# Optimization experiments

Measured on AMD Instinct MI355X. Metric: run time of the kernel, lower is better.

The kernel has to match this reference:

```python
import jax, jax.numpy as jnp
import numpy as np

ALPHA = 0.2
WINDOW = 64
HEADS = 2

def _mhsa(x, qkv_W, qkv_b, out_W, out_b):
    # x: (M, w, C)
    M, w, C = x.shape
    hd = C // HEADS
    qkv = (x @ qkv_W + qkv_b).reshape(M, w, 3, HEADS, hd)
    q, k, v = qkv[:, :, 0], qkv[:, :, 1], qkv[:, :, 2]  # (M, w, H, hd)
    att = jnp.einsum('mqhd,mkhd->mhqk', q, k) * (hd ** -0.5)
    att = jax.nn.softmax(att, axis=-1)
    o = jnp.einsum('mhqk,mkhd->mqhd', att, v).reshape(M, w, C)
    return o @ out_W + out_b

def _block_pass(x, qkv_W, qkv_b, out_W, out_b):
    # x: (B*L, L, C) -> windowed attention along axis 1
    BL, L, C = x.shape
    pad = (-L) % WINDOW
    if pad > 0:
        x = jnp.pad(x, ((0, 0), (0, pad), (0, 0)))
    Lp = L + pad
    nblk = Lp // WINDOW
    xb = x.reshape(BL * nblk, WINDOW, C)
    xb = _mhsa(xb, qkv_W, qkv_b, out_W, out_b)
    return xb.reshape(BL, Lp, C)[:, :L, :]

def setup_inputs() -> dict:
    key = jax.random.key(0)
    ks = jax.random.split(key, 12)
    s = 0.02
    d = {
        'single': jax.random.normal(ks[0], (1, 512, 256), jnp.float32),
        'pair': jax.random.normal(ks[1], (1, 512, 512, 128), jnp.float32),
        'film_W1': jax.random.normal(ks[2], (512, 128), jnp.float32) * s,
        'film_b1': jnp.zeros((128,), jnp.float32),
        'film_W2': jax.random.normal(ks[3], (128, 256), jnp.float32) * s,
        'film_b2': jnp.zeros((256,), jnp.float32),
        'red_W1': jax.random.normal(ks[4], (128, 64), jnp.float32) * s,
        'red_b1': jnp.zeros((64,), jnp.float32),
        'red_W2': jax.random.normal(ks[5], (64, 32), jnp.float32) * s,
        'red_b2': jnp.zeros((32,), jnp.float32),
        'qkv_W': jax.random.normal(ks[6], (32, 96), jnp.float32) * s,
        'qkv_b': jnp.zeros((96,), jnp.float32),
        'out_W': jax.random.normal(ks[7], (32, 32), jnp.float32) * s,
        'out_b': jnp.zeros((32,), jnp.float32),
        'head_W1': jax.random.normal(ks[8], (32, 64), jnp.float32) * s,
        'head_b1': jnp.zeros((64,), jnp.float32),
        'head_W2': jax.random.normal(ks[9], (64, 1), jnp.float32) * s,
        'head_b2': jnp.zeros((1,), jnp.float32),
    }
    return d

def reference(single, pair, film_W1, film_b1, film_W2, film_b2,
              red_W1, red_b1, red_W2, red_b2,
              qkv_W, qkv_b, out_W, out_b,
              head_W1, head_b1, head_W2, head_b2):
    B, L, Ds = single.shape
    pair_dim = pair.shape[-1]
    # ResidualFiLM: concat([Si,Sj]) @ W1 == Si @ W1[:Ds] + Sj @ W1[Ds:]
    pi = single @ film_W1[:Ds]   # (B, L, hidden)
    pj = single @ film_W1[Ds:]   # (B, L, hidden)
    h = jax.nn.relu(pi[:, :, None, :] + pj[:, None, :, :] + film_b1)  # (B,L,L,hidden)
    x = h @ film_W2 + film_b2    # (B,L,L,2*pair_dim)
    gamma = 1.0 + ALPHA * jnp.tanh(x[..., :pair_dim])
    beta = ALPHA * jnp.tanh(x[..., pair_dim:])
    pair2 = gamma * pair + beta
    # pair_reduce: Linear -> GELU(exact) -> Linear
    pair2 = jax.nn.gelu(pair2 @ red_W1 + red_b1, approximate=False) @ red_W2 + red_b2  # (B,L,L,32)
    C = pair2.shape[-1]
    # row pass
    row = _block_pass(pair2.reshape(B * L, L, C), qkv_W, qkv_b, out_W, out_b)
    row = row.reshape(B, L, L, C)
    # col pass (attend along first L axis)
    col = _block_pass(row.transpose(0, 2, 1, 3).reshape(B * L, L, C), qkv_W, qkv_b, out_W, out_b)
    pair3 = col.reshape(B, L, L, C).transpose(0, 2, 1, 3)
    # head
    logits = (jax.nn.relu(pair3 @ head_W1 + head_b1) @ head_W2 + head_b2)[..., 0]
    return jax.nn.sigmoid(logits)  # (B,L,L)
```

## Files before the change

### kernel.cpp

```cpp
#include <hip/hip_runtime.h>
#include <hip/hip_bf16.h>
#include <math.h>

typedef unsigned short u16;
typedef u16 u16x8 __attribute__((ext_vector_type(8)));
typedef u16 u16x4 __attribute__((ext_vector_type(4)));
typedef __bf16 bf16x8 __attribute__((ext_vector_type(8)));
typedef float f32x4 __attribute__((ext_vector_type(4)));

__device__ __forceinline__ u16 f2bf(float f) {
    return __builtin_bit_cast(u16, (__bf16)f);
}
__device__ __forceinline__ float ftanh(float x) {
    const float e = __expf(2.f * x);
    return 1.f - 2.f * __builtin_amdgcn_rcpf(e + 1.f);
}
__device__ __forceinline__ float fgelu(float x) {
    const float u = 0.7978845608028654f * x * (1.f + 0.044715f * x * x);
    return 0.5f * x * (1.f + ftanh(u));
}

#define MFMA16(A, B, C) __builtin_amdgcn_mfma_f32_16x16x32_bf16( \
    __builtin_bit_cast(bf16x8, A), __builtin_bit_cast(bf16x8, B), C, 0, 0, 0)

#define BARRIER() do { \
    asm volatile("s_waitcnt lgkmcnt(0)" ::: "memory"); \
    __builtin_amdgcn_s_barrier(); \
    __builtin_amdgcn_sched_barrier(0); \
} while (0)

__global__ __launch_bounds__(256) void k_prep(
    const float* __restrict__ fW2, const float* __restrict__ rW1,
    const float* __restrict__ rW2, const float* __restrict__ qW,
    const float* __restrict__ oW,
    u16* __restrict__ W2T, u16* __restrict__ rW1T, u16* __restrict__ rW2T,
    u16* __restrict__ qWT, u16* __restrict__ oWT)
{
    const int idx = blockIdx.x * 256 + threadIdx.x;
    if (idx < 256 * 128) {
        const int c = idx >> 7, k = idx & 127;
        W2T[idx] = f2bf(fW2[k * 256 + c]);
    }
    const int i2 = idx - 32768;
    if (i2 >= 0 && i2 < 64 * 128) {
        const int d = i2 >> 7, k = i2 & 127;
        rW1T[i2] = f2bf(rW1[k * 64 + d]);
    }
    const int i3 = idx - 40960;
    if (i3 >= 0 && i3 < 32 * 64) {
        const int e = i3 >> 6, d = i3 & 63;
        rW2T[i3] = f2bf(rW2[d * 32 + e]);
    }
    const int i4 = idx - 43008;
    if (i4 >= 0 && i4 < 96 * 32) {
        const int col = i4 >> 5, c = i4 & 31;
        qWT[i4] = f2bf(qW[c * 96 + col]);
    }
    const int i5 = idx - 46080;
    if (i5 >= 0 && i5 < 32 * 32) {
        const int oc = i5 >> 5, d = i5 & 31;
        oWT[i5] = f2bf(oW[d * 32 + oc]);
    }
}

__global__ __launch_bounds__(256) void k_pipj(const float* __restrict__ single,
                                              const float* __restrict__ fW1,
                                              const float* __restrict__ fb1,
                                              float* __restrict__ pi,
                                              float* __restrict__ pj) {
    const int i = blockIdx.x;
    const int t = threadIdx.x;
    const int sel = t >> 7;
    const int c = t & 127;
    const float* srow = single + i * 256;
    const float* w = fW1 + sel * 256 * 128 + c;
    float acc = 0.f;
    for (int k = 0; k < 256; ++k) acc += srow[k] * w[k * 128];
    if (sel == 0) acc += fb1[c];
    float* dst = sel ? pj : pi;
    dst[i * 128 + c] = acc;
}

__global__ __launch_bounds__(256) void k_film_red_mfma(
    const float* __restrict__ pair,
    const float* __restrict__ pi,
    const float* __restrict__ pj,
    const u16*   __restrict__ W2T,
    const float* __restrict__ fb2,
    const u16*   __restrict__ rW1T,
    const float* __restrict__ rb1,
    const u16*   __restrict__ rW2T,
    const float* __restrict__ rb2,
    float* __restrict__ out)
{
    __shared__ __align__(16) char hs [32 * 256];
    __shared__ __align__(16) char p2s[32 * 256];
    __shared__ __align__(16) char t1s[32 * 128];

    const int t = threadIdx.x;
    const int lane = t & 63, w = t >> 6;
    const int g = lane >> 4, ln = lane & 15;
    const int i = blockIdx.x >> 4;
    const int j0 = (blockIdx.x & 15) * 32;

    const int jj = t >> 3;
    const int k0 = (t & 7) * 16;
    const float* pir = pi + i * 128 + k0;
    const float* pjr = pj + (j0 + jj) * 128 + k0;
    f32x4 pv[4], qv[4];
#pragma unroll
    for (int q4 = 0; q4 < 4; ++q4) {
        pv[q4] = *(const f32x4*)(pir + 4 * q4);
        qv[q4] = *(const f32x4*)(pjr + 4 * q4);
    }

    u16x8 af1[4][4];
#pragma unroll
    for (int a = 0; a < 4; ++a)
#pragma unroll
        for (int ks = 0; ks < 4; ++ks)
            af1[a][ks] = *(const u16x8*)(W2T + ((w + 4 * a) * 16 + ln) * 128 + ks * 32 + g * 8);

    f32x4 pr[2][2];
#pragma unroll
    for (int a2 = 0; a2 < 2; ++a2)
#pragma unroll
        for (int nt = 0; nt < 2; ++nt) {
            const int j = nt * 16 + ln;
            const int c0 = (w + 4 * a2) * 16 + g * 4;
            pr[a2][nt] = *(const f32x4*)(pair + ((long)(i * 512 + j0 + j)) * 128 + c0);
        }

    {
        u16x8 pk0, pk1;
#pragma unroll
        for (int e = 0; e < 8; ++e) {
            const float v0 = pv[e >> 2][e & 3] + qv[e >> 2][e & 3];
            const float v1 = pv[2 + (e >> 2)][e & 3] + qv[2 + (e >> 2)][e & 3];
            pk0[e] = f2bf(fmaxf(v0, 0.f));
            pk1[e] = f2bf(fmaxf(v1, 0.f));
        }
        const int sw = (jj & 7) << 4;
        *(u16x8*)(hs + jj * 256 + ((2 * k0) ^ sw)) = pk0;
        *(u16x8*)(hs + jj * 256 + ((2 * (k0 + 8)) ^ sw)) = pk1;
    }
    BARRIER();

    f32x4 acc[4][2] = {};
#pragma unroll
    for (int ks = 0; ks < 4; ++ks) {
        u16x8 b0, b1;
        {
            const int jA = ln, jB = 16 + ln;
            const int k = ks * 32 + g * 8;
            b0 = *(const u16x8*)(hs + jA * 256 + ((2 * k) ^ ((jA & 7) << 4)));
            b1 = *(const u16x8*)(hs + jB * 256 + ((2 * k) ^ ((jB & 7) << 4)));
        }
#pragma unroll
        for (int a = 0; a < 4; ++a) {
            acc[a][0] = MFMA16(af1[a][ks], b0, acc[a][0]);
            acc[a][1] = MFMA16(af1[a][ks], b1, acc[a][1]);
        }
    }

    u16x8 af2[4];
#pragma unroll
    for (int ks = 0; ks < 4; ++ks)
        af2[ks] = *(const u16x8*)(rW1T + (w * 16 + ln) * 128 + ks * 32 + g * 8);

#pragma unroll
    for (int a2 = 0; a2 < 2; ++a2) {
        const int c0 = (w + 4 * a2) * 16 + g * 4;
        const f32x4 blo = *(const f32x4*)(fb2 + c0);
        const f32x4 bhi = *(const f32x4*)(fb2 + 128 + c0);
#pragma unroll
        for (int nt = 0; nt < 2; ++nt) {
            u16x4 pb;
#pragma unroll
            for (int r = 0; r < 4; ++r) {
                const float xlo = acc[a2][nt][r] + blo[r];
                const float xhi = acc[a2 + 2][nt][r] + bhi[r];
                const float gam = 1.f + 0.2f * ftanh(xlo);
                const float bet = 0.2f * ftanh(xhi);
                pb[r] = f2bf(gam * pr[a2][nt][r] + bet);
            }
            const int j = nt * 16 + ln;
            *(u16x4*)(p2s + j * 256 + ((2 * c0) ^ ((j & 7) << 4))) = pb;
        }
    }
    BARRIER();

    const int mt3 = w >> 1, nt3 = w & 1;
    u16x8 a3[2];
#pragma unroll
    for (int ks = 0; ks < 2; ++ks)
        a3[ks] = *(const u16x8*)(rW2T + (mt3 * 16 + ln) * 64 + ks * 32 + g * 8);

    f32x4 acc2[2] = {};
#pragma unroll
    for (int ks = 0; ks < 4; ++ks) {
        const int k = ks * 32 + g * 8;
        const int jA = ln, jB = 16 + ln;
        const u16x8 b0 = *(const u16x8*)(p2s + jA * 256 + ((2 * k) ^ ((jA & 7) << 4)));
        const u16x8 b1 = *(const u16x8*)(p2s + jB * 256 + ((2 * k) ^ ((jB & 7) << 4)));
        acc2[0] = MFMA16(af2[ks], b0, acc2[0]);
        acc2[1] = MFMA16(af2[ks], b1, acc2[1]);
    }

    {
        const int d0 = w * 16 + g * 4;
        const f32x4 rb = *(const f32x4*)(rb1 + d0);
#pragma unroll
        for (int nt = 0; nt < 2; ++nt) {
            u16x4 tb;
#pragma unroll
            for (int r = 0; r < 4; ++r)
                tb[r] = f2bf(fgelu(acc2[nt][r] + rb[r]));
            const int j = nt * 16 + ln;
            *(u16x4*)(t1s + j * 128 + ((2 * d0) ^ ((j & 7) << 4))) = tb;
        }
    }
    BARRIER();

    {
        f32x4 acc3 = {};
#pragma unroll
        for (int ks = 0; ks < 2; ++ks) {
            const int j = nt3 * 16 + ln;
            const int k = ks * 32 + g * 8;
            const u16x8 b3 = *(const u16x8*)(t1s + j * 128 + ((2 * k) ^ ((j & 7) << 4)));
            acc3 = MFMA16(a3[ks], b3, acc3);
        }
        const int e0 = mt3 * 16 + g * 4;
        const f32x4 rb = *(const f32x4*)(rb2 + e0);
        f32x4 o;
#pragma unroll
        for (int r = 0; r < 4; ++r) o[r] = acc3[r] + rb[r];
        const int j = nt3 * 16 + ln;
        *(f32x4*)(out + ((long)(i * 512 + j0 + j)) * 32 + e0) = o;
    }
}

__global__ __launch_bounds__(128) void k_attn_mfma(
    const float* __restrict__ in, float* __restrict__ outbuf,
    const u16* __restrict__ qWT,
    const float* __restrict__ qb,
    const u16* __restrict__ oWT,
    const float* __restrict__ ob,
    const int col_pass)
{
    __shared__ u16 Xs[64][40];
    __shared__ u16 qks[64][72];
    __shared__ u16 vPs[2][16][72];

    const int t = threadIdx.x;
    const int lane = t & 63, w = t >> 6;
    const int g = lane >> 4, ln = lane & 15;
    const int p = w;

    const int id = blockIdx.x;
    long base; int stride;
    if (col_pass) { stride = 512 * 32; base = (long)((id & 7) * 64) * (512 * 32) + (long)(id >> 3) * 32; }
    else          { stride = 32;       base = ((long)(id >> 3) * 512 + (id & 7) * 64) * 32; }

    u16x8 bw[4];
#pragma unroll
    for (int nt = 0; nt < 4; ++nt)
        bw[nt] = *(const u16x8*)(qWT + (nt * 16 + ln) * 32 + g * 8);
    const u16x8 av = *(const u16x8*)(qWT + (64 + p * 16 + ln) * 32 + g * 8);
    float qbias[4];
#pragma unroll
    for (int nt = 0; nt < 4; ++nt) qbias[nt] = qb[nt * 16 + ln];
    const f32x4 vb = *(const f32x4*)(qb + 64 + p * 16 + g * 4);

    {
        const int tok = t >> 1, c0 = (t & 1) * 16;
        const float* src = in + base + (long)tok * stride + c0;
        u16x8 a, b;
#pragma unroll
        for (int e = 0; e < 8; ++e) { a[e] = f2bf(src[e]); b[e] = f2bf(src[8 + e]); }
        *(u16x8*)&Xs[tok][c0] = a;
        *(u16x8*)&Xs[tok][c0 + 8] = b;
    }
    BARRIER();

    {
        u16x8 bx[4];
#pragma unroll
        for (int nt = 0; nt < 4; ++nt)
            bx[nt] = *(const u16x8*)&Xs[nt * 16 + ln][g * 8];
#pragma unroll
        for (int s = 0; s < 2; ++s) {
            const u16x8 ax = bx[2 * p + s];
            f32x4 qa[4] = {};
#pragma unroll
            for (int nt = 0; nt < 4; ++nt)
                qa[nt] = MFMA16(ax, bw[nt], qa[nt]);
#pragma unroll
            for (int nt = 0; nt < 4; ++nt)
#pragma unroll
                for (int r = 0; r < 4; ++r)
                    qks[(2 * p + s) * 16 + g * 4 + r][nt * 16 + ln] = f2bf(qa[nt][r] + qbias[nt]);
        }
#pragma unroll
        for (int nt = 0; nt < 4; ++nt) {
            f32x4 va = MFMA16(av, bx[nt], ((f32x4){0.f, 0.f, 0.f, 0.f}));
            const int tok = nt * 16 + ln;
            const int kk = (tok & 32) | ((tok & 12) << 1) | ((tok & 16) >> 2) | (tok & 3);
#pragma unroll
            for (int r = 0; r < 4; ++r)
                vPs[p][g * 4 + r][kk] = f2bf(va[r] + vb[r]);
        }
    }
    BARRIER();

    {
        const int h = w;
        const u16x8 zero8 = {};
        u16x8 bq[4];
#pragma unroll
        for (int nt = 0; nt < 4; ++nt)
            bq[nt] = (g < 2) ? *(const u16x8*)&qks[nt * 16 + ln][h * 16 + g * 8] : zero8;
        f32x4 s_[4][4] = {};
#pragma unroll
        for (int mt = 0; mt < 4; ++mt) {
            const u16x8 ak = (g < 2) ? *(const u16x8*)&qks[mt * 16 + ln][32 + h * 16 + g * 8] : zero8;
#pragma unroll
            for (int nt = 0; nt < 4; ++nt)
                s_[mt][nt] = MFMA16(ak, bq[nt], s_[mt][nt]);
        }
        u16x8 paf[4][2];
#pragma unroll
        for (int nt = 0; nt < 4; ++nt) {
            float mx = -1e30f;
#pragma unroll
            for (int mt = 0; mt < 4; ++mt)
#pragma unroll
                for (int r = 0; r < 4; ++r) {
                    s_[mt][nt][r] *= 0.25f;
                    mx = fmaxf(mx, s_[mt][nt][r]);
                }
            mx = fmaxf(mx, __shfl_xor(mx, 16));
            mx = fmaxf(mx, __shfl_xor(mx, 32));
            float sum = 0.f;
#pragma unroll
            for (int mt = 0; mt < 4; ++mt)
#pragma unroll
                for (int r = 0; r < 4; ++r) {
                    const float e_ = __expf(s_[mt][nt][r] - mx);
                    s_[mt][nt][r] = e_;
                    sum += e_;
                }
            sum += __shfl_xor(sum, 16);
            sum += __shfl_xor(sum, 32);
            const float inv = __builtin_amdgcn_rcpf(sum);
#pragma unroll
            for (int s2 = 0; s2 < 2; ++s2) {
                u16x8 pk;
#pragma unroll
                for (int e = 0; e < 8; ++e)
                    pk[e] = f2bf(s_[2 * s2 + (e >> 2)][nt][e & 3] * inv);
                paf[nt][s2] = pk;
            }
        }
        u16x8 bv[2];
#pragma unroll
        for (int s2 = 0; s2 < 2; ++s2)
            bv[s2] = *(const u16x8*)&vPs[h][ln][s2 * 32 + g * 8];
        f32x4 oacc[4] = {};
#pragma unroll
        for (int nt = 0; nt < 4; ++nt)
#pragma unroll
            for (int s2 = 0; s2 < 2; ++s2)
                oacc[nt] = MFMA16(paf[nt][s2], bv[s2], oacc[nt]);
#pragma unroll
        for (int nt = 0; nt < 4; ++nt)
#pragma unroll
            for (int r = 0; r < 4; ++r)
                Xs[nt * 16 + g * 4 + r][h * 16 + ln] = f2bf(oacc[nt][r]);
    }
    BARRIER();

    {
        u16x8 bo[2];
#pragma unroll
        for (int nt = 0; nt < 2; ++nt)
            bo[nt] = *(const u16x8*)(oWT + (nt * 16 + ln) * 32 + g * 8);
        float ob2[2];
#pragma unroll
        for (int nt = 0; nt < 2; ++nt) ob2[nt] = ob[nt * 16 + ln];
#pragma unroll
        for (int s = 0; s < 2; ++s) {
            const u16x8 ao = *(const u16x8*)&Xs[(2 * p + s) * 16 + ln][g * 8];
            f32x4 oa[2] = {};
#pragma unroll
            for (int nt = 0; nt < 2; ++nt)
                oa[nt] = MFMA16(ao, bo[nt], oa[nt]);
#pragma unroll
            for (int nt = 0; nt < 2; ++nt) {
                const int oc = nt * 16 + ln;
#pragma unroll
                for (int r = 0; r < 4; ++r) {
                    const int tok = (2 * p + s) * 16 + g * 4 + r;
                    outbuf[base + (long)tok * stride + oc] = oa[nt][r] + ob2[nt];
                }
            }
        }
    }
}

__global__ __launch_bounds__(256) void k_head(
    const float* __restrict__ p3,
    const float* __restrict__ hW1,
    const float* __restrict__ hb1,
    const float* __restrict__ hW2,
    const float* __restrict__ hb2,
    float* __restrict__ outp)
{
    __shared__ float w1s[32][64];
    __shared__ float w2s[64];
    __shared__ float b1s[64];
    const int t = threadIdx.x;
    for (int u = t; u < 2048; u += 256) w1s[u >> 6][u & 63] = hW1[u];
    if (t < 64) { w2s[t] = hW2[t]; b1s[t] = hb1[t]; }
    __syncthreads();
    const float hb2v = hb2[0];

    const long idx = (long)blockIdx.x * 256 + t;
    const float4* xp = (const float4*)(p3 + idx * 32);
    float x[32];
#pragma unroll
    for (int q4 = 0; q4 < 8; ++q4) {
        const float4 v = xp[q4];
        x[q4 * 4 + 0] = v.x; x[q4 * 4 + 1] = v.y;
        x[q4 * 4 + 2] = v.z; x[q4 * 4 + 3] = v.w;
    }
    float logit = hb2v;
    for (int d = 0; d < 64; ++d) {
        float s = b1s[d];
#pragma unroll
        for (int c = 0; c < 32; ++c) s += x[c] * w1s[c][d];
        s = s > 0.f ? s : 0.f;
        logit += s * w2s[d];
    }
    outp[idx] = __builtin_amdgcn_rcpf(1.f + __expf(-logit));
}

extern "C" void kernel_launch(void* const* d_in, const int* in_sizes, int n_in,
                              void* d_out, int out_size, void* d_ws, size_t ws_size,
                              hipStream_t stream) {
    (void)in_sizes; (void)n_in; (void)out_size; (void)ws_size;
    const float* single = (const float*)d_in[0];
    const float* pair   = (const float*)d_in[1];
    const float* fW1 = (const float*)d_in[2];
    const float* fb1 = (const float*)d_in[3];
    const float* fW2 = (const float*)d_in[4];
    const float* fb2 = (const float*)d_in[5];
    const float* rW1 = (const float*)d_in[6];
    const float* rb1 = (const float*)d_in[7];
    const float* rW2 = (const float*)d_in[8];
    const float* rb2 = (const float*)d_in[9];
    const float* qW  = (const float*)d_in[10];
    const float* qb  = (const float*)d_in[11];
    const float* oW  = (const float*)d_in[12];
    const float* ob  = (const float*)d_in[13];
    const float* hW1 = (const float*)d_in[14];
    const float* hb1 = (const float*)d_in[15];
    const float* hW2 = (const float*)d_in[16];
    const float* hb2 = (const float*)d_in[17];
    float* outp = (float*)d_out;

    char* ws = (char*)d_ws;
    float* pi   = (float*)ws;
    float* pj   = (float*)(ws + 256 * 1024);
    u16*   W2T  = (u16*)(ws + 512 * 1024);
    u16*   rW1T = (u16*)(ws + 576 * 1024);
    u16*   rW2T = (u16*)(ws + 592 * 1024);
    u16*   qWTd = (u16*)(ws + 608 * 1024);
    u16*   oWTd = (u16*)(ws + 616 * 1024);
    float* bufA = (float*)(ws + 1024 * 1024);
    float* bufB = (float*)(ws + 1024 * 1024 + 33554432);

    k_prep<<<184, 256, 0, stream>>>(fW2, rW1, rW2, qW, oW, W2T, rW1T, rW2T, qWTd, oWTd);
    k_pipj<<<512, 256, 0, stream>>>(single, fW1, fb1, pi, pj);
    k_film_red_mfma<<<8192, 256, 0, stream>>>(pair, pi, pj, W2T, fb2,
                                              rW1T, rb1, rW2T, rb2, bufA);
    k_attn_mfma<<<4096, 128, 0, stream>>>(bufA, bufB, qWTd, qb, oWTd, ob, 0);
    k_attn_mfma<<<4096, 128, 0, stream>>>(bufB, bufA, qWTd, qb, oWTd, ob, 1);
    k_head<<<1024, 256, 0, stream>>>(bufA, hW1, hb1, hW2, hb2, outp);
}
```

Measured before the change: 403.3 us.

## Store intermediates in bf16, persist film tiles, batch attention windows, MFMA head

The intermediate pair activations between stages are now stored as bf16 instead of fp32, which halves global traffic for the attention passes and the head. The film/reduce kernel processes four j-tiles per block and prefetches the next tile's pair and pj data while the current tile computes. The attention kernel handles two windows per 256-thread block and reads bf16 input directly into registers. The head becomes an MFMA kernel using a bf16-transposed W1. The trade-off is extra bf16 rounding on the intermediates, plus higher register pressure from the prefetching.

Result: faster. 342.8 us (-15.0%).

```diff
diff --git a/kernel.cpp b/kernel.cpp
--- a/kernel.cpp
+++ b/kernel.cpp
@@ -32,9 +32,9 @@
 __global__ __launch_bounds__(256) void k_prep(
     const float* __restrict__ fW2, const float* __restrict__ rW1,
     const float* __restrict__ rW2, const float* __restrict__ qW,
-    const float* __restrict__ oW,
+    const float* __restrict__ oW, const float* __restrict__ hW1,
     u16* __restrict__ W2T, u16* __restrict__ rW1T, u16* __restrict__ rW2T,
-    u16* __restrict__ qWT, u16* __restrict__ oWT)
+    u16* __restrict__ qWT, u16* __restrict__ oWT, u16* __restrict__ hW1T)
 {
     const int idx = blockIdx.x * 256 + threadIdx.x;
     if (idx < 256 * 128) {
@@ -60,6 +60,11 @@
     if (i5 >= 0 && i5 < 32 * 32) {
         const int oc = i5 >> 5, d = i5 & 31;
         oWT[i5] = f2bf(oW[d * 32 + oc]);
+    }
+    const int i6 = idx - 47104;
+    if (i6 >= 0 && i6 < 64 * 32) {
+        const int d = i6 >> 5, c = i6 & 31;
+        hW1T[i6] = f2bf(hW1[c * 64 + d]);
     }
 }
 
@@ -91,7 +96,7 @@
     const float* __restrict__ rb1,
     const u16*   __restrict__ rW2T,
     const float* __restrict__ rb2,
-    float* __restrict__ out)
+    u16* __restrict__ out)
 {
     __shared__ __align__(16) char hs [32 * 256];
     __shared__ __align__(16) char p2s[32 * 256];
@@ -100,195 +105,213 @@
     const int t = threadIdx.x;
     const int lane = t & 63, w = t >> 6;
     const int g = lane >> 4, ln = lane & 15;
-    const int i = blockIdx.x >> 4;
-    const int j0 = (blockIdx.x & 15) * 32;
-
-    const int jj = t >> 3;
-    const int k0 = (t & 7) * 16;
-    const float* pir = pi + i * 128 + k0;
-    const float* pjr = pj + (j0 + jj) * 128 + k0;
-    f32x4 pv[4], qv[4];
-#pragma unroll
-    for (int q4 = 0; q4 < 4; ++q4) {
-        pv[q4] = *(const f32x4*)(pir + 4 * q4);
-        qv[q4] = *(const f32x4*)(pjr + 4 * q4);
-    }
-
+    const int i = blockIdx.x >> 2;
+    const int jbase = (blockIdx.x & 3) * 128;
+    const int jj = t >> 3, k0 = (t & 7) * 16;
+    const int mt3 = w >> 1, nt3 = w & 1;
+
+    f32x4 pv[4];
+    {
+        const float* pir = pi + i * 128 + k0;
+#pragma unroll
+        for (int q4 = 0; q4 < 4; ++q4) pv[q4] = *(const f32x4*)(pir + 4 * q4);
+    }
     u16x8 af1[4][4];
 #pragma unroll
     for (int a = 0; a < 4; ++a)
 #pragma unroll
         for (int ks = 0; ks < 4; ++ks)
             af1[a][ks] = *(const u16x8*)(W2T + ((w + 4 * a) * 16 + ln) * 128 + ks * 32 + g * 8);
-
-    f32x4 pr[2][2];
-#pragma unroll
-    for (int a2 = 0; a2 < 2; ++a2)
-#pragma unroll
-        for (int nt = 0; nt < 2; ++nt) {
-            const int j = nt * 16 + ln;
-            const int c0 = (w + 4 * a2) * 16 + g * 4;
-            pr[a2][nt] = *(const f32x4*)(pair + ((long)(i * 512 + j0 + j)) * 128 + c0);
-        }
-
-    {
-        u16x8 pk0, pk1;
-#pragma unroll
-        for (int e = 0; e < 8; ++e) {
-            const float v0 = pv[e >> 2][e & 3] + qv[e >> 2][e & 3];
-            const float v1 = pv[2 + (e >> 2)][e & 3] + qv[2 + (e >> 2)][e & 3];
-            pk0[e] = f2bf(fmaxf(v0, 0.f));
-            pk1[e] = f2bf(fmaxf(v1, 0.f));
-        }
-        const int sw = (jj & 7) << 4;
-        *(u16x8*)(hs + jj * 256 + ((2 * k0) ^ sw)) = pk0;
-        *(u16x8*)(hs + jj * 256 + ((2 * (k0 + 8)) ^ sw)) = pk1;
-    }
-    BARRIER();
-
-    f32x4 acc[4][2] = {};
-#pragma unroll
-    for (int ks = 0; ks < 4; ++ks) {
-        u16x8 b0, b1;
-        {
-            const int jA = ln, jB = 16 + ln;
-            const int k = ks * 32 + g * 8;
-            b0 = *(const u16x8*)(hs + jA * 256 + ((2 * k) ^ ((jA & 7) << 4)));
-            b1 = *(const u16x8*)(hs + jB * 256 + ((2 * k) ^ ((jB & 7) << 4)));
-        }
-#pragma unroll
-        for (int a = 0; a < 4; ++a) {
-            acc[a][0] = MFMA16(af1[a][ks], b0, acc[a][0]);
-            acc[a][1] = MFMA16(af1[a][ks], b1, acc[a][1]);
-        }
-    }
-
     u16x8 af2[4];
 #pragma unroll
     for (int ks = 0; ks < 4; ++ks)
         af2[ks] = *(const u16x8*)(rW1T + (w * 16 + ln) * 128 + ks * 32 + g * 8);
-
+    u16x8 a3[2];
+#pragma unroll
+    for (int ks = 0; ks < 2; ++ks)
+        a3[ks] = *(const u16x8*)(rW2T + (mt3 * 16 + ln) * 64 + ks * 32 + g * 8);
+    f32x4 blo2[2], bhi2[2];
 #pragma unroll
     for (int a2 = 0; a2 < 2; ++a2) {
         const int c0 = (w + 4 * a2) * 16 + g * 4;
-        const f32x4 blo = *(const f32x4*)(fb2 + c0);
-        const f32x4 bhi = *(const f32x4*)(fb2 + 128 + c0);
-#pragma unroll
-        for (int nt = 0; nt < 2; ++nt) {
-            u16x4 pb;
-#pragma unroll
-            for (int r = 0; r < 4; ++r) {
-                const float xlo = acc[a2][nt][r] + blo[r];
-                const float xhi = acc[a2 + 2][nt][r] + bhi[r];
-                const float gam = 1.f + 0.2f * ftanh(xlo);
-                const float bet = 0.2f * ftanh(xhi);
-                pb[r] = f2bf(gam * pr[a2][nt][r] + bet);
-            }
-            const int j = nt * 16 + ln;
-            *(u16x4*)(p2s + j * 256 + ((2 * c0) ^ ((j & 7) << 4))) = pb;
-        }
-    }
-    BARRIER();
-
-    const int mt3 = w >> 1, nt3 = w & 1;
-    u16x8 a3[2];
-#pragma unroll
-    for (int ks = 0; ks < 2; ++ks)
-        a3[ks] = *(const u16x8*)(rW2T + (mt3 * 16 + ln) * 64 + ks * 32 + g * 8);
-
-    f32x4 acc2[2] = {};
-#pragma unroll
-    for (int ks = 0; ks < 4; ++ks) {
-        const int k = ks * 32 + g * 8;
-        const int jA = ln, jB = 16 + ln;
-        const u16x8 b0 = *(const u16x8*)(p2s + jA * 256 + ((2 * k) ^ ((jA & 7) << 4)));
-        const u16x8 b1 = *(const u16x8*)(p2s + jB * 256 + ((2 * k) ^ ((jB & 7) << 4)));
-        acc2[0] = MFMA16(af2[ks], b0, acc2[0]);
-        acc2[1] = MFMA16(af2[ks], b1, acc2[1]);
-    }
-
-    {
-        const int d0 = w * 16 + g * 4;
-        const f32x4 rb = *(const f32x4*)(rb1 + d0);
-#pragma unroll
-        for (int nt = 0; nt < 2; ++nt) {
-            u16x4 tb;
-#pragma unroll
-            for (int r = 0; r < 4; ++r)
-                tb[r] = f2bf(fgelu(acc2[nt][r] + rb[r]));
-            const int j = nt * 16 + ln;
-            *(u16x4*)(t1s + j * 128 + ((2 * d0) ^ ((j & 7) << 4))) = tb;
-        }
-    }
-    BARRIER();
-
-    {
-        f32x4 acc3 = {};
-#pragma unroll
-        for (int ks = 0; ks < 2; ++ks) {
+        blo2[a2] = *(const f32x4*)(fb2 + c0);
+        bhi2[a2] = *(const f32x4*)(fb2 + 128 + c0);
+    }
+    const f32x4 rbv  = *(const f32x4*)(rb1 + w * 16 + g * 4);
+    const f32x4 rb2v = *(const f32x4*)(rb2 + mt3 * 16 + g * 4);
+
+    auto loadQ = [&](int J0, f32x4 (&QV)[4]) {
+        const float* pjr = pj + (long)(J0 + jj) * 128 + k0;
+#pragma unroll
+        for (int q4 = 0; q4 < 4; ++q4) QV[q4] = *(const f32x4*)(pjr + 4 * q4);
+    };
+    auto loadP = [&](int J0, f32x4 (&PR)[2][2]) {
+#pragma unroll
+        for (int a2 = 0; a2 < 2; ++a2)
+#pragma unroll
+            for (int nt = 0; nt < 2; ++nt)
+                PR[a2][nt] = *(const f32x4*)(pair + ((long)(i * 512 + J0 + nt * 16 + ln)) * 128
+                                             + (w + 4 * a2) * 16 + g * 4);
+    };
+
+    auto tile = [&](int J0, f32x4 (&QV)[4], f32x4 (&PR)[2][2],
+                    int JN, f32x4 (&QN)[4], f32x4 (&PN)[2][2], bool pref) {
+        {
+            u16x8 pk0, pk1;
+#pragma unroll
+            for (int e = 0; e < 8; ++e) {
+                const float v0 = pv[e >> 2][e & 3] + QV[e >> 2][e & 3];
+                const float v1 = pv[2 + (e >> 2)][e & 3] + QV[2 + (e >> 2)][e & 3];
+                pk0[e] = f2bf(fmaxf(v0, 0.f));
+                pk1[e] = f2bf(fmaxf(v1, 0.f));
+            }
+            const int sw = (jj & 7) << 4;
+            *(u16x8*)(hs + jj * 256 + ((2 * k0) ^ sw)) = pk0;
+            *(u16x8*)(hs + jj * 256 + ((2 * (k0 + 8)) ^ sw)) = pk1;
+        }
+        if (pref) { loadQ(JN, QN); loadP(JN, PN); }
+        BARRIER();
+
+        f32x4 acc[4][2] = {};
+#pragma unroll
+        for (int ks = 0; ks < 4; ++ks) {
+            const int k = ks * 32 + g * 8;
+            const int jA = ln, jB = 16 + ln;
+            const u16x8 b0 = *(const u16x8*)(hs + jA * 256 + ((2 * k) ^ ((jA & 7) << 4)));
+            const u16x8 b1 = *(const u16x8*)(hs + jB * 256 + ((2 * k) ^ ((jB & 7) << 4)));
+#pragma unroll
+            for (int a = 0; a < 4; ++a) {
+                acc[a][0] = MFMA16(af1[a][ks], b0, acc[a][0]);
+                acc[a][1] = MFMA16(af1[a][ks], b1, acc[a][1]);
+            }
+        }
+
+#pragma unroll
+        for (int a2 = 0; a2 < 2; ++a2) {
+            const int c0 = (w + 4 * a2) * 16 + g * 4;
+#pragma unroll
+            for (int nt = 0; nt < 2; ++nt) {
+                u16x4 pb;
+#pragma unroll
+                for (int r = 0; r < 4; ++r) {
+                    const float xlo = acc[a2][nt][r] + blo2[a2][r];
+                    const float xhi = acc[a2 + 2][nt][r] + bhi2[a2][r];
+                    const float gam = 1.f + 0.2f * ftanh(xlo);
+                    const float bet = 0.2f * ftanh(xhi);
+                    pb[r] = f2bf(gam * PR[a2][nt][r] + bet);
+                }
+                const int j = nt * 16 + ln;
+                *(u16x4*)(p2s + j * 256 + ((2 * c0) ^ ((j & 7) << 4))) = pb;
+            }
+        }
+        BARRIER();
+
+        f32x4 acc2[2] = {};
+#pragma unroll
+        for (int ks = 0; ks < 4; ++ks) {
+            const int k = ks * 32 + g * 8;
+            const int jA = ln, jB = 16 + ln;
+            const u16x8 b0 = *(const u16x8*)(p2s + jA * 256 + ((2 * k) ^ ((jA & 7) << 4)));
+            const u16x8 b1 = *(const u16x8*)(p2s + jB * 256 + ((2 * k) ^ ((jB & 7) << 4)));
+            acc2[0] = MFMA16(af2[ks], b0, acc2[0]);
+            acc2[1] = MFMA16(af2[ks], b1, acc2[1]);
+        }
+        {
+            const int d0 = w * 16 + g * 4;
+#pragma unroll
+            for (int nt = 0; nt < 2; ++nt) {
+                u16x4 tb;
+#pragma unroll
+                for (int r = 0; r < 4; ++r)
+                    tb[r] = f2bf(fgelu(acc2[nt][r] + rbv[r]));
+                const int j = nt * 16 + ln;
+                *(u16x4*)(t1s + j * 128 + ((2 * d0) ^ ((j & 7) << 4))) = tb;
+            }
+        }
+        BARRIER();
+
+        {
+            f32x4 acc3 = {};
+#pragma unroll
+            for (int ks = 0; ks < 2; ++ks) {
+                const int j = nt3 * 16 + ln;
+                const int k = ks * 32 + g * 8;
+                const u16x8 b3 = *(const u16x8*)(t1s + j * 128 + ((2 * k) ^ ((j & 7) << 4)));
+                acc3 = MFMA16(a3[ks], b3, acc3);
+            }
+            const int e0 = mt3 * 16 + g * 4;
+            u16x4 o;
+#pragma unroll
+            for (int r = 0; r < 4; ++r) o[r] = f2bf(acc3[r] + rb2v[r]);
             const int j = nt3 * 16 + ln;
-            const int k = ks * 32 + g * 8;
-            const u16x8 b3 = *(const u16x8*)(t1s + j * 128 + ((2 * k) ^ ((j & 7) << 4)));
-            acc3 = MFMA16(a3[ks], b3, acc3);
-        }
-        const int e0 = mt3 * 16 + g * 4;
-        const f32x4 rb = *(const f32x4*)(rb2 + e0);
-        f32x4 o;
-#pragma unroll
-        for (int r = 0; r < 4; ++r) o[r] = acc3[r] + rb[r];
-        const int j = nt3 * 16 + ln;
-        *(f32x4*)(out + ((long)(i * 512 + j0 + j)) * 32 + e0) = o;
-    }
-}
-
-__global__ __launch_bounds__(128) void k_attn_mfma(
-    const float* __restrict__ in, float* __restrict__ outbuf,
+            *(u16x4*)(out + ((long)(i * 512 + J0 + j)) * 32 + e0) = o;
+        }
+    };
+
+    f32x4 qvA[4], qvB[4], prA[2][2], prB[2][2];
+    loadQ(jbase, qvA); loadP(jbase, prA);
+    tile(jbase,      qvA, prA, jbase + 32, qvB, prB, true);
+    tile(jbase + 32, qvB, prB, jbase + 64, qvA, prA, true);
+    tile(jbase + 64, qvA, prA, jbase + 96, qvB, prB, true);
+    tile(jbase + 96, qvB, prB, jbase,      qvA, prA, false);
+}
+
+__global__ __launch_bounds__(256) void k_attn_mfma(
+    const u16* __restrict__ in, u16* __restrict__ outbuf,
     const u16* __restrict__ qWT,
     const float* __restrict__ qb,
     const u16* __restrict__ oWT,
     const float* __restrict__ ob,
     const int col_pass)
 {
-    __shared__ u16 Xs[64][40];
-    __shared__ u16 qks[64][72];
-    __shared__ u16 vPs[2][16][72];
+    __shared__ __align__(16) char smem[18432 + 9216 + 10240];
+    u16 (*qks)[64][72]     = (u16(*)[64][72])smem;
+    u16 (*vPs)[2][16][72]  = (u16(*)[2][16][72])(smem + 18432);
+    u16 (*osb)[64][40]     = (u16(*)[64][40])(smem + 27648);
+    u16 (*fout)[64][40]    = (u16(*)[64][40])smem;
 
     const int t = threadIdx.x;
     const int lane = t & 63, w = t >> 6;
     const int g = lane >> 4, ln = lane & 15;
-    const int p = w;
-
-    const int id = blockIdx.x;
-    long base; int stride;
-    if (col_pass) { stride = 512 * 32; base = (long)((id & 7) * 64) * (512 * 32) + (long)(id >> 3) * 32; }
-    else          { stride = 32;       base = ((long)(id >> 3) * 512 + (id & 7) * 64) * 32; }
+    const int wnd = w >> 1, sub = w & 1;
+
+    const int wid0 = blockIdx.x * 2;
+    long base0, base1; int stride;
+    if (col_pass) {
+        stride = 512 * 32;
+        base0 = (long)((wid0 & 7) * 64) * (512 * 32) + (long)(wid0 >> 3) * 32;
+        base1 = (long)(((wid0 + 1) & 7) * 64) * (512 * 32) + (long)((wid0 + 1) >> 3) * 32;
+    } else {
+        stride = 32;
+        base0 = ((long)(wid0 >> 3) * 512 + (wid0 & 7) * 64) * 32;
+        base1 = ((long)((wid0 + 1) >> 3) * 512 + ((wid0 + 1) & 7) * 64) * 32;
+    }
+    const long myb = wnd ? base1 : base0;
 
     u16x8 bw[4];
 #pragma unroll
     for (int nt = 0; nt < 4; ++nt)
         bw[nt] = *(const u16x8*)(qWT + (nt * 16 + ln) * 32 + g * 8);
-    const u16x8 av = *(const u16x8*)(qWT + (64 + p * 16 + ln) * 32 + g * 8);
+    const u16x8 av = *(const u16x8*)(qWT + (64 + sub * 16 + ln) * 32 + g * 8);
+    u16x8 bo[2];
+#pragma unroll
+    for (int nt = 0; nt < 2; ++nt)
+        bo[nt] = *(const u16x8*)(oWT + (nt * 16 + ln) * 32 + g * 8);
     float qbias[4];
 #pragma unroll
     for (int nt = 0; nt < 4; ++nt) qbias[nt] = qb[nt * 16 + ln];
-    const f32x4 vb = *(const f32x4*)(qb + 64 + p * 16 + g * 4);
+    const f32x4 vb = *(const f32x4*)(qb + 64 + sub * 16 + g * 4);
+    float ob2[2];
+#pragma unroll
+    for (int nt = 0; nt < 2; ++nt) ob2[nt] = ob[nt * 16 + ln];
+
+    u16x8 bx[4];
+#pragma unroll
+    for (int nt = 0; nt < 4; ++nt)
+        bx[nt] = *(const u16x8*)(in + myb + (long)(nt * 16 + ln) * stride + g * 8);
 
     {
-        const int tok = t >> 1, c0 = (t & 1) * 16;
-        const float* src = in + base + (long)tok * stride + c0;
-        u16x8 a, b;
-#pragma unroll
-        for (int e = 0; e < 8; ++e) { a[e] = f2bf(src[e]); b[e] = f2bf(src[8 + e]); }
-        *(u16x8*)&Xs[tok][c0] = a;
-        *(u16x8*)&Xs[tok][c0 + 8] = b;
-    }
-    BARRIER();
-
-    {
-        u16x8 bx[4];
-#pragma unroll
-        for (int nt = 0; nt < 4; ++nt)
-            bx[nt] = *(const u16x8*)&Xs[nt * 16 + ln][g * 8];
+        const int p = sub;
 #pragma unroll
         for (int s = 0; s < 2; ++s) {
             const u16x8 ax = bx[2 * p + s];
@@ -300,7 +323,7 @@
             for (int nt = 0; nt < 4; ++nt)
 #pragma unroll
                 for (int r = 0; r < 4; ++r)
-                    qks[(2 * p + s) * 16 + g * 4 + r][nt * 16 + ln] = f2bf(qa[nt][r] + qbias[nt]);
+                    qks[wnd][(2 * p + s) * 16 + g * 4 + r][nt * 16 + ln] = f2bf(qa[nt][r] + qbias[nt]);
         }
 #pragma unroll
         for (int nt = 0; nt < 4; ++nt) {
@@ -309,141 +332,145 @@
             const int kk = (tok & 32) | ((tok & 12) << 1) | ((tok & 16) >> 2) | (tok & 3);
 #pragma unroll
             for (int r = 0; r < 4; ++r)
-                vPs[p][g * 4 + r][kk] = f2bf(va[r] + vb[r]);
+                vPs[wnd][p][g * 4 + r][kk] = f2bf(va[r] + vb[r]);
         }
     }
     BARRIER();
 
     {
-        const int h = w;
+        const int h = sub;
         const u16x8 zero8 = {};
-        u16x8 bq[4];
-#pragma unroll
-        for (int nt = 0; nt < 4; ++nt)
-            bq[nt] = (g < 2) ? *(const u16x8*)&qks[nt * 16 + ln][h * 16 + g * 8] : zero8;
-        f32x4 s_[4][4] = {};
-#pragma unroll
-        for (int mt = 0; mt < 4; ++mt) {
-            const u16x8 ak = (g < 2) ? *(const u16x8*)&qks[mt * 16 + ln][32 + h * 16 + g * 8] : zero8;
-#pragma unroll
-            for (int nt = 0; nt < 4; ++nt)
-                s_[mt][nt] = MFMA16(ak, bq[nt], s_[mt][nt]);
-        }
-        u16x8 paf[4][2];
-#pragma unroll
-        for (int nt = 0; nt < 4; ++nt) {
-            float mx = -1e30f;
-#pragma unroll
-            for (int mt = 0; mt < 4; ++mt)
-#pragma unroll
-                for (int r = 0; r < 4; ++r) {
-                    s_[mt][nt][r] *= 0.25f;
-                    mx = fmaxf(mx, s_[mt][nt][r]);
+        u16x8 bv[2];
+#pragma unroll
+        for (int s2 = 0; s2 < 2; ++s2)
+            bv[s2] = *(const u16x8*)&vPs[wnd][h][ln][s2 * 32 + g * 8];
+#pragma unroll
+        for (int half = 0; half < 2; ++half) {
+            u16x8 bq[2];
+#pragma unroll
+            for (int q2 = 0; q2 < 2; ++q2) {
+                const int nt = half * 2 + q2;
+                bq[q2] = (g < 2) ? *(const u16x8*)&qks[wnd][nt * 16 + ln][h * 16 + g * 8] : zero8;
+            }
+            f32x4 s_[4][2] = {};
+#pragma unroll
+            for (int mt = 0; mt < 4; ++mt) {
+                const u16x8 ak = (g < 2) ? *(const u16x8*)&qks[wnd][mt * 16 + ln][32 + h * 16 + g * 8] : zero8;
+#pragma unroll
+                for (int q2 = 0; q2 < 2; ++q2)
+                    s_[mt][q2] = MFMA16(ak, bq[q2], s_[mt][q2]);
+            }
+#pragma unroll
+            for (int q2 = 0; q2 < 2; ++q2) {
+                float mx = -1e30f;
+#pragma unroll
+                for (int mt = 0; mt < 4; ++mt)
+#pragma unroll
+                    for (int r = 0; r < 4; ++r) {
+                        s_[mt][q2][r] *= 0.25f;
+                        mx = fmaxf(mx, s_[mt][q2][r]);
+                    }
+                mx = fmaxf(mx, __shfl_xor(mx, 16));
+                mx = fmaxf(mx, __shfl_xor(mx, 32));
+                float sum = 0.f;
+#pragma unroll
+                for (int mt = 0; mt < 4; ++mt)
+#pragma unroll
+                    for (int r = 0; r < 4; ++r) {
+                        const float e_ = __expf(s_[mt][q2][r] - mx);
+                        s_[mt][q2][r] = e_;
+                        sum += e_;
+                    }
+                sum += __shfl_xor(sum, 16);
+                sum += __shfl_xor(sum, 32);
+                const float inv = __builtin_amdgcn_rcpf(sum);
+                f32x4 oacc = {};
+#pragma unroll
+                for (int s2 = 0; s2 < 2; ++s2) {
+                    u16x8 pk;
+#pragma unroll
+                    for (int e = 0; e < 8; ++e)
+                        pk[e] = f2bf(s_[2 * s2 + (e >> 2)][q2][e & 3] * inv);
+                    oacc = MFMA16(pk, bv[s2], oacc);
                 }
-            mx = fmaxf(mx, __shfl_xor(mx, 16));
-            mx = fmaxf(mx, __shfl_xor(mx, 32));
-            float sum = 0.f;
-#pragma unroll
-            for (int mt = 0; mt < 4; ++mt)
-#pragma unroll
-                for (int r = 0; r < 4; ++r) {
-                    const float e_ = __expf(s_[mt][nt][r] - mx);
-                    s_[mt][nt][r] = e_;
-                    sum += e_;
-                }
-            sum += __shfl_xor(sum, 16);
-            sum += __shfl_xor(sum, 32);
-            const float inv = __builtin_amdgcn_rcpf(sum);
-#pragma unroll
-            for (int s2 = 0; s2 < 2; ++s2) {
-                u16x8 pk;
-#pragma unroll
-                for (int e = 0; e < 8; ++e)
-                    pk[e] = f2bf(s_[2 * s2 + (e >> 2)][nt][e & 3] * inv);
-                paf[nt][s2] = pk;
-            }
-        }
-        u16x8 bv[2];
-#pragma unroll
-        for (int s2 = 0; s2 < 2; ++s2)
-            bv[s2] = *(const u16x8*)&vPs[h][ln][s2 * 32 + g * 8];
-        f32x4 oacc[4] = {};
-#pragma unroll
-        for (int nt = 0; nt < 4; ++nt)
-#pragma unroll
-            for (int s2 = 0; s2 < 2; ++s2)
-                oacc[nt] = MFMA16(paf[nt][s2], bv[s2], oacc[nt]);
-#pragma unroll
-        for (int nt = 0; nt < 4; ++nt)
-#pragma unroll
-            for (int r = 0; r < 4; ++r)
-                Xs[nt * 16 + g * 4 + r][h * 16 + ln] = f2bf(oacc[nt][r]);
+                const int ntg = half * 2 + q2;
+#pragma unroll
+                for (int r = 0; r < 4; ++r)
+                    osb[wnd][ntg * 16 + g * 4 + r][h * 16 + ln] = f2bf(oacc[r]);
+            }
+        }
     }
     BARRIER();
 
     {
-        u16x8 bo[2];
-#pragma unroll
-        for (int nt = 0; nt < 2; ++nt)
-            bo[nt] = *(const u16x8*)(oWT + (nt * 16 + ln) * 32 + g * 8);
-        float ob2[2];
-#pragma unroll
-        for (int nt = 0; nt < 2; ++nt) ob2[nt] = ob[nt * 16 + ln];
+        const int p = sub;
 #pragma unroll
         for (int s = 0; s < 2; ++s) {
-            const u16x8 ao = *(const u16x8*)&Xs[(2 * p + s) * 16 + ln][g * 8];
+            const u16x8 ao = *(const u16x8*)&osb[wnd][(2 * p + s) * 16 + ln][g * 8];
             f32x4 oa[2] = {};
 #pragma unroll
             for (int nt = 0; nt < 2; ++nt)
                 oa[nt] = MFMA16(ao, bo[nt], oa[nt]);
 #pragma unroll
-            for (int nt = 0; nt < 2; ++nt) {
-                const int oc = nt * 16 + ln;
-#pragma unroll
-                for (int r = 0; r < 4; ++r) {
-                    const int tok = (2 * p + s) * 16 + g * 4 + r;
-                    outbuf[base + (long)tok * stride + oc] = oa[nt][r] + ob2[nt];
-                }
-            }
-        }
-    }
-}
-
-__global__ __launch_bounds__(256) void k_head(
-    const float* __restrict__ p3,
-    const float* __restrict__ hW1,
+            for (int nt = 0; nt < 2; ++nt)
+#pragma unroll
+                for (int r = 0; r < 4; ++r)
+                    fout[wnd][(2 * p + s) * 16 + g * 4 + r][nt * 16 + ln] = f2bf(oa[nt][r] + ob2[nt]);
+        }
+    }
+    BARRIER();
+
+    {
+        const int wnd2 = t >> 7, rr = t & 127, tok = rr >> 1, hf = rr & 1;
+        const long b2 = wnd2 ? base1 : base0;
+        const u16x8 v0 = *(const u16x8*)&fout[wnd2][tok][hf * 16];
+        const u16x8 v1 = *(const u16x8*)&fout[wnd2][tok][hf * 16 + 8];
+        u16* dst = outbuf + b2 + (long)tok * stride + hf * 16;
+        *(u16x8*)dst = v0;
+        *(u16x8*)(dst + 8) = v1;
+    }
+}
+
+__global__ __launch_bounds__(256) void k_head_mfma(
+    const u16* __restrict__ p3,
+    const u16* __restrict__ hW1T,
     const float* __restrict__ hb1,
     const float* __restrict__ hW2,
     const float* __restrict__ hb2,
     float* __restrict__ outp)
 {
-    __shared__ float w1s[32][64];
-    __shared__ float w2s[64];
-    __shared__ float b1s[64];
-    const int t = threadIdx.x;
-    for (int u = t; u < 2048; u += 256) w1s[u >> 6][u & 63] = hW1[u];
-    if (t < 64) { w2s[t] = hW2[t]; b1s[t] = hb1[t]; }
-    __syncthreads();
+    const int t = threadIdx.x, lane = t & 63, w = t >> 6;
+    const int g = lane >> 4, ln = lane & 15;
+    u16x8 aH[4]; f32x4 b1v[4], w2v[4];
+#pragma unroll
+    for (int mt = 0; mt < 4; ++mt) {
+        aH[mt]  = *(const u16x8*)(hW1T + (mt * 16 + ln) * 32 + g * 8);
+        b1v[mt] = *(const f32x4*)(hb1 + mt * 16 + g * 4);
+        w2v[mt] = *(const f32x4*)(hW2 + mt * 16 + g * 4);
+    }
     const float hb2v = hb2[0];
-
-    const long idx = (long)blockIdx.x * 256 + t;
-    const float4* xp = (const float4*)(p3 + idx * 32);
-    float x[32];
-#pragma unroll
-    for (int q4 = 0; q4 < 8; ++q4) {
-        const float4 v = xp[q4];
-        x[q4 * 4 + 0] = v.x; x[q4 * 4 + 1] = v.y;
-        x[q4 * 4 + 2] = v.z; x[q4 * 4 + 3] = v.w;
-    }
-    float logit = hb2v;
-    for (int d = 0; d < 64; ++d) {
-        float s = b1s[d];
-#pragma unroll
-        for (int c = 0; c < 32; ++c) s += x[c] * w1s[c][d];
-        s = s > 0.f ? s : 0.f;
-        logit += s * w2s[d];
-    }
-    outp[idx] = __builtin_amdgcn_rcpf(1.f + __expf(-logit));
+    const long tok0 = (long)blockIdx.x * 256 + w * 64;
+#pragma unroll
+    for (int it = 0; it < 4; ++it) {
+        const long tb = tok0 + it * 16;
+        const u16x8 bxh = *(const u16x8*)(p3 + (tb + ln) * 32 + g * 8);
+        float partial = 0.f;
+#pragma unroll
+        for (int mt = 0; mt < 4; ++mt) {
+            f32x4 y = MFMA16(aH[mt], bxh, ((f32x4){0.f, 0.f, 0.f, 0.f}));
+#pragma unroll
+            for (int r = 0; r < 4; ++r) {
+                const float v = fmaxf(y[r] + b1v[mt][r], 0.f);
+                partial += v * w2v[mt][r];
+            }
+        }
+        partial += __shfl_xor(partial, 16);
+        partial += __shfl_xor(partial, 32);
+        if (g == 0) {
+            const float logit = partial + hb2v;
+            outp[tb + ln] = __builtin_amdgcn_rcpf(1.f + __expf(-logit));
+        }
+    }
 }
 
 extern "C" void kernel_launch(void* const* d_in, const int* in_sizes, int n_in,
@@ -471,21 +498,23 @@
     float* outp = (float*)d_out;
 
     char* ws = (char*)d_ws;
-    float* pi   = (float*)ws;
-    float* pj   = (float*)(ws + 256 * 1024);
-    u16*   W2T  = (u16*)(ws + 512 * 1024);
-    u16*   rW1T = (u16*)(ws + 576 * 1024);
-    u16*   rW2T = (u16*)(ws + 592 * 1024);
-    u16*   qWTd = (u16*)(ws + 608 * 1024);
-    u16*   oWTd = (u16*)(ws + 616 * 1024);
-    float* bufA = (float*)(ws + 1024 * 1024);
-    float* bufB = (float*)(ws + 1024 * 1024 + 33554432);
-
-    k_prep<<<184, 256, 0, stream>>>(fW2, rW1, rW2, qW, oW, W2T, rW1T, rW2T, qWTd, oWTd);
+    float* pi    = (float*)ws;
+    float* pj    = (float*)(ws + 256 * 1024);
+    u16*   W2T   = (u16*)(ws + 512 * 1024);
+    u16*   rW1T  = (u16*)(ws + 576 * 1024);
+    u16*   rW2T  = (u16*)(ws + 592 * 1024);
+    u16*   qWTd  = (u16*)(ws + 608 * 1024);
+    u16*   oWTd  = (u16*)(ws + 616 * 1024);
+    u16*   hW1Td = (u16*)(ws + 620 * 1024);
+    u16*   bufA  = (u16*)(ws + 1024 * 1024);
+    u16*   bufB  = (u16*)(ws + 1024 * 1024 + 17 * 1024 * 1024);
+
+    k_prep<<<192, 256, 0, stream>>>(fW2, rW1, rW2, qW, oW, hW1,
+                                    W2T, rW1T, rW2T, qWTd, oWTd, hW1Td);
     k_pipj<<<512, 256, 0, stream>>>(single, fW1, fb1, pi, pj);
-    k_film_red_mfma<<<8192, 256, 0, stream>>>(pair, pi, pj, W2T, fb2,
+    k_film_red_mfma<<<2048, 256, 0, stream>>>(pair, pi, pj, W2T, fb2,
                                               rW1T, rb1, rW2T, rb2, bufA);
-    k_attn_mfma<<<4096, 128, 0, stream>>>(bufA, bufB, qWTd, qb, oWTd, ob, 0);
-    k_attn_mfma<<<4096, 128, 0, stream>>>(bufB, bufA, qWTd, qb, oWTd, ob, 1);
-    k_head<<<1024, 256, 0, stream>>>(bufA, hW1, hb1, hW2, hb2, outp);
-}
+    k_attn_mfma<<<2048, 256, 0, stream>>>(bufA, bufB, qWTd, qb, oWTd, ob, 0);
+    k_attn_mfma<<<2048, 256, 0, stream>>>(bufB, bufA, qWTd, qb, oWTd, ob, 1);
+    k_head_mfma<<<1024, 256, 0, stream>>>(bufA, hW1Td, hb1, hW2, hb2, outp);
+}
```
